# Performance work log

Hardware: AMD Instinct MI355X
Metric: run time of the kernel (lower is better)

The kernel has to match this reference:

```python
import jax, jax.numpy as jnp
import numpy as np

CHUNK = 128
EPS = 1e-6


def setup_inputs() -> dict:
    key = jax.random.key(0)
    k1, k2, k3 = jax.random.split(key, 3)
    B, H, N, D, E = 4, 8, 4096, 64, 64
    q = jax.random.uniform(k1, (B, H, N, D), dtype=jnp.float32)
    k = jax.random.uniform(k2, (B, H, N, D), dtype=jnp.float32)
    v = jax.random.normal(k3, (B, H, N, E), dtype=jnp.float32)
    return {"q": q, "k": k, "v": v, "inferrring_states": 1}


def reference(q, k, v, inferrring_states):
    # infer_hidden_states path: chunked causal linear attention with carried state.
    B, H, N, D = q.shape
    E = v.shape[-1]
    nc = N // CHUNK
    # [nc, B, H, CHUNK, *] for scan over chunks
    qc = jnp.moveaxis(q.reshape(B, H, nc, CHUNK, D), 2, 0)
    kc = jnp.moveaxis(k.reshape(B, H, nc, CHUNK, D), 2, 0)
    vc = jnp.moveaxis(v.reshape(B, H, nc, CHUNK, E), 2, 0)

    Z0 = jnp.zeros((B, H, 1, D), dtype=q.dtype)        # running sum of k
    S0 = jnp.zeros((B, H, 1, D, E), dtype=q.dtype)     # running sum of k v^T

    def step(carry, qkv):
        Z, S = carry
        qi, ki, vi = qkv
        k_cumsum = Z + jnp.cumsum(ki, axis=-2)                      # [B,H,C,D]
        D_inv = 1.0 / jnp.einsum('bhnd,bhnd->bhn', qi, k_cumsum + EPS)
        context = jnp.einsum('bhnd,bhne->bhnde', ki, vi)            # [B,H,C,D,E]
        ctx_cumsum = S + jnp.cumsum(context, axis=-3)
        out = jnp.einsum('bhnde,bhnd,bhn->bhne', ctx_cumsum, qi, D_inv)
        new_carry = (k_cumsum[:, :, -1:], ctx_cumsum[:, :, -1:])
        return new_carry, out

    (Z, S), outs = jax.lax.scan(step, (Z0, S0), (qc, kc, vc))
    out = jnp.moveaxis(outs, 0, 2).reshape(B, H, N, E)
    # states: Z=[B,H,D], S=[B,H,D,E]
    return out, Z[:, :, 0], S[:, :, 0]
```

## Files before the change

### kernel.cpp

```cpp
#include <hip/hip_runtime.h>


#define CHUNKSZ 128
#define DD 64
#define EE 64
#define NC 32
#define NBH 32
#define NSEQ 4096
#define EPSV 1e-6f
#define OUT0 (NBH * NSEQ * EE)
#define KV_ELEMS (NBH * NC * DD * EE)

typedef short bf16x8 __attribute__((ext_vector_type(8)));
typedef short bf16x4 __attribute__((ext_vector_type(4)));
typedef float f32x4  __attribute__((ext_vector_type(4)));

__device__ __forceinline__ unsigned short f2bf(float f) {
    union { float f; unsigned u; } x; x.f = f;
    unsigned u = x.u + 0x7FFFu + ((x.u >> 16) & 1u);
    return (unsigned short)(u >> 16);
}
__device__ __forceinline__ float bf2f(unsigned short s) {
    union { unsigned u; float f; } x; x.u = ((unsigned)s) << 16;
    return x.f;
}

__global__ __launch_bounds__(256) void la_phase1(
    const float* __restrict__ k, const float* __restrict__ v,
    unsigned short* __restrict__ kvT, float* __restrict__ ks)
{
    const int blk = blockIdx.x;
    const int bh = blk / NC, c = blk % NC;
    const size_t rowbase = (size_t)bh * NSEQ + (size_t)c * CHUNKSZ;

    __shared__ alignas(16) unsigned short kT[CHUNKSZ * DD];
    __shared__ alignas(16) unsigned short vT[CHUNKSZ * EE];
    __shared__ float ksp[4][DD];

    char* kb = (char*)kT;
    char* vb = (char*)vT;

    const int t = threadIdx.x;
    const int w = t >> 6, l = t & 63;
    const int lg = l >> 4, lm = l & 15;
    const int col = t & 63;

    float kpart = 0.f;
#pragma unroll
    for (int pass = 0; pass < 4; ++pass) {
        const int mg = w + 4 * pass;
        const float* kp = k + (rowbase + mg * 8) * DD + col;
        const float* vp = v + (rowbase + mg * 8) * EE + col;
        float kf[8], vf[8];
#pragma unroll
        for (int j = 0; j < 8; ++j) kf[j] = kp[(size_t)j * DD];
#pragma unroll
        for (int j = 0; j < 8; ++j) vf[j] = vp[(size_t)j * EE];
        bf16x8 ku, vu;
#pragma unroll
        for (int j = 0; j < 8; ++j) {
            kpart += kf[j];
            ku[j] = (short)f2bf(kf[j]);
            vu[j] = (short)f2bf(vf[j]);
        }
        *(bf16x8*)(kb + mg * 1024 + col * 16) = ku;
        *(bf16x8*)(vb + mg * 1024 + col * 16) = vu;
    }
    ksp[w][col] = kpart;
    __syncthreads();

    f32x4 acc[4] = {};
#pragma unroll
    for (int kk = 0; kk < 4; ++kk) {
        bf16x8 aK = *(bf16x8*)(kb + (lg + 4 * kk) * 1024 + (16 * w + lm) * 16);
#pragma unroll
        for (int ei = 0; ei < 4; ++ei) {
            bf16x8 bV = *(bf16x8*)(vb + (lg + 4 * kk) * 1024 + (16 * ei + lm) * 16);
            acc[ei] = __builtin_amdgcn_mfma_f32_16x16x32_bf16(aK, bV, acc[ei], 0, 0, 0);
        }
    }
    unsigned short* kvout = kvT + (size_t)(bh * NC + c) * DD * EE;
#pragma unroll
    for (int ei = 0; ei < 4; ++ei) {
        bf16x4 u;
        u[0] = (short)f2bf(acc[ei][0]); u[1] = (short)f2bf(acc[ei][1]);
        u[2] = (short)f2bf(acc[ei][2]); u[3] = (short)f2bf(acc[ei][3]);
        *(bf16x4*)(kvout + (16 * ei + lm) * DD + 16 * w + 4 * lg) = u;
    }
    if (t < DD)
        ks[(size_t)(bh * NC + c) * DD + t] = ksp[0][t] + ksp[1][t] + ksp[2][t] + ksp[3][t];
}

__global__ __launch_bounds__(64) void la_phase2(
    unsigned short* __restrict__ kvT, float* __restrict__ ks, float* __restrict__ out)
{
    const int bid = blockIdx.x, t = threadIdx.x;
    if (bid < 256) {
        const int gid = bid * 64 + t;
        const int bh = gid >> 9;
        const int g = gid & 511;
        unsigned short* base = kvT + (size_t)bh * (NC * DD * EE) + (size_t)g * 8;
        bf16x8 vals[NC];
#pragma unroll
        for (int c = 0; c < NC; ++c)
            vals[c] = *(const bf16x8*)(base + (size_t)c * (DD * EE));
        float run[8] = {};
#pragma unroll
        for (int c = 0; c < NC; ++c) {
            bf16x8 pr;
#pragma unroll
            for (int j = 0; j < 8; ++j) pr[j] = (short)f2bf(run[j]);
            *(bf16x8*)(base + (size_t)c * (DD * EE)) = pr;
#pragma unroll
            for (int j = 0; j < 8; ++j) run[j] += bf2f((unsigned short)vals[c][j]);
        }
        const int e = g >> 3, d0 = (g & 7) * 8;
        float* Sout = out + OUT0 + NBH * DD + (size_t)bh * DD * EE;
#pragma unroll
        for (int j = 0; j < 8; ++j)
            Sout[(size_t)(d0 + j) * EE + e] = run[j];
    } else {
        const int tid = (bid - 256) * 64 + t;
        const int bh = tid >> 6, d = tid & 63;
        float vals[NC];
#pragma unroll
        for (int c = 0; c < NC; ++c)
            vals[c] = ks[(size_t)(bh * NC + c) * DD + d];
        float run = 0.f;
#pragma unroll
        for (int c = 0; c < NC; ++c) {
            float x = vals[c];
            ks[(size_t)(bh * NC + c) * DD + d] = run;
            run += x;
        }
        out[OUT0 + tid] = run;
    }
}

__global__ __launch_bounds__(256) void la_phase3(
    const float* __restrict__ q, const float* __restrict__ k,
    const float* __restrict__ v, const unsigned short* __restrict__ kvT,
    const float* __restrict__ ks, float* __restrict__ out)
{
    const int blk = blockIdx.x;
    const int bh = blk / NC, c = blk % NC;
    const size_t rowbase = (size_t)bh * NSEQ + (size_t)c * CHUNKSZ;

    __shared__ alignas(16) unsigned short k_lds[CHUNKSZ * DD];
    __shared__ alignas(16) unsigned short v_lds[CHUNKSZ * EE];
    __shared__ float zi_lds[DD];

    char* kb = (char*)k_lds;
    char* vb = (char*)v_lds;

    const int t  = threadIdx.x;
    const int w  = t >> 6;
    const int l  = t & 63;
    const int lg = l >> 4;
    const int lm = l & 15;

    {
        const float4* kg = (const float4*)(k + rowbase * DD);
#pragma unroll
        for (int i = 0; i < 8; ++i) {
            int idx = t + i * 256;
            int m = idx >> 4, c4 = idx & 15;
            float4 f = kg[idx];
            bf16x4 u;
            u[0] = (short)f2bf(f.x); u[1] = (short)f2bf(f.y);
            u[2] = (short)f2bf(f.z); u[3] = (short)f2bf(f.w);
            int byt = m * 128 + ((c4 * 8) ^ ((m & 7) << 4));
            *(bf16x4*)(kb + byt) = u;
        }
    }
    {
        const int col = t & 63;
#pragma unroll
        for (int pass = 0; pass < 4; ++pass) {
            const int mg = (t >> 6) + 4 * pass;
            const float* vp = v + (rowbase + mg * 8) * EE + col;
            float vf[8];
#pragma unroll
            for (int j = 0; j < 8; ++j) vf[j] = vp[(size_t)j * EE];
            bf16x8 u;
#pragma unroll
            for (int j = 0; j < 8; ++j) u[j] = (short)f2bf(vf[j]);
            *(bf16x8*)(vb + mg * 1024 + col * 16) = u;
        }
    }
    const unsigned short* stc = kvT + (size_t)(bh * NC + c) * DD * EE;
    bf16x8 b_st[4][2];
#pragma unroll
    for (int ei = 0; ei < 4; ++ei)
#pragma unroll
        for (int kk = 0; kk < 2; ++kk)
            b_st[ei][kk] = *(const bf16x8*)(stc + (size_t)(16 * ei + lm) * DD + 8 * lg + 32 * kk);

    if (t < DD) zi_lds[t] = ks[(size_t)(bh * NC + c) * DD + t];
    __syncthreads();

    const int src1 = 32 * (lg & 1) + lm;
    const int src2 = src1 + 16;
    const int par  = lg >> 1;

#pragma unroll
    for (int ni2 = 0; ni2 < 2; ++ni2) {
        const int ni = ni2 ? (7 - w) : w;
        const int n = 16 * ni + lm;
        const int kmax = (ni >> 1) + 1;

        bf16x8 aq[2];
        {
            const float* qrow = q + (rowbase + n) * DD;
#pragma unroll
            for (int kk = 0; kk < 2; ++kk) {
                const float4* p = (const float4*)(qrow + 8 * lg + 32 * kk);
                float4 f0 = p[0], f1 = p[1];
                bf16x8 u;
                u[0] = (short)f2bf(f0.x); u[1] = (short)f2bf(f0.y);
                u[2] = (short)f2bf(f0.z); u[3] = (short)f2bf(f0.w);
                u[4] = (short)f2bf(f1.x); u[5] = (short)f2bf(f1.y);
                u[6] = (short)f2bf(f1.z); u[7] = (short)f2bf(f1.w);
                aq[kk] = u;
            }
        }

        unsigned a_s[4][4];
#pragma unroll
        for (int b = 0; b < 4; ++b) {
            a_s[b][0] = 0; a_s[b][1] = 0; a_s[b][2] = 0; a_s[b][3] = 0;
        }

        float rsum = 0.f;
#pragma unroll
        for (int mi = 0; mi < 8; ++mi) {
            if (mi <= ni) {
                f32x4 cc = {0.f, 0.f, 0.f, 0.f};
                const int mrow = 16 * mi + lm;
#pragma unroll
                for (int kk = 0; kk < 2; ++kk) {
                    int byt = mrow * 128 + (((8 * lg + 32 * kk) * 2) ^ ((mrow & 7) << 4));
                    bf16x8 ak = *(bf16x8*)(kb + byt);
                    cc = __builtin_amdgcn_mfma_f32_16x16x32_bf16(ak, aq[kk], cc, 0, 0, 0);
                }
                const int m0 = 16 * mi + 4 * lg;
                float v0 = (m0 + 0 <= n) ? cc[0] : 0.f;
                float v1 = (m0 + 1 <= n) ? cc[1] : 0.f;
                float v2 = (m0 + 2 <= n) ? cc[2] : 0.f;
                float v3 = (m0 + 3 <= n) ? cc[3] : 0.f;
                rsum += (v0 + v1) + (v2 + v3);
                unsigned p_lo = (unsigned)f2bf(v0) | ((unsigned)f2bf(v1) << 16);
                unsigned p_hi = (unsigned)f2bf(v2) | ((unsigned)f2bf(v3) << 16);
                unsigned w0 = (unsigned)__shfl((int)p_lo, src1);
                unsigned w1 = (unsigned)__shfl((int)p_hi, src1);
                unsigned w2 = (unsigned)__shfl((int)p_lo, src2);
                unsigned w3 = (unsigned)__shfl((int)p_hi, src2);
                const bool take = (par == (mi & 1));
                const int b = mi >> 1;
                a_s[b][0] = take ? w0 : a_s[b][0];
                a_s[b][1] = take ? w1 : a_s[b][1];
                a_s[b][2] = take ? w2 : a_s[b][2];
                a_s[b][3] = take ? w3 : a_s[b][3];
            }
        }

        float qz = 0.f, qs = 0.f;
#pragma unroll
        for (int kk = 0; kk < 2; ++kk) {
#pragma unroll
            for (int i = 0; i < 8; ++i) {
                float qf = bf2f((unsigned short)aq[kk][i]);
                qz += qf * zi_lds[8 * lg + 32 * kk + i];
                qs += qf;
            }
        }
        float part = rsum + qz + EPSV * qs;
        part += __shfl_xor(part, 16);
        part += __shfl_xor(part, 32);
        const float dinv = 1.f / part;

        f32x4 acc[4];
#pragma unroll
        for (int ei = 0; ei < 4; ++ei) {
            f32x4 cc = {0.f, 0.f, 0.f, 0.f};
            const int e = 16 * ei + lm;
            cc = __builtin_amdgcn_mfma_f32_16x16x32_bf16(aq[0], b_st[ei][0], cc, 0, 0, 0);
            cc = __builtin_amdgcn_mfma_f32_16x16x32_bf16(aq[1], b_st[ei][1], cc, 0, 0, 0);
#pragma unroll
            for (int kk = 0; kk < 4; ++kk) {
                if (kk < kmax) {
                    union { unsigned u[4]; bf16x8 f; } as;
                    as.u[0] = a_s[kk][0]; as.u[1] = a_s[kk][1];
                    as.u[2] = a_s[kk][2]; as.u[3] = a_s[kk][3];
                    int bytB = (lg + 4 * kk) * 1024 + e * 16;
                    bf16x8 bv = *(bf16x8*)(vb + bytB);
                    cc = __builtin_amdgcn_mfma_f32_16x16x32_bf16(as.f, bv, cc, 0, 0, 0);
                }
            }
            acc[ei] = cc;
        }

#pragma unroll
        for (int r = 0; r < 4; ++r) {
            float dr = __shfl(dinv, 4 * lg + r);
            const int nr = 16 * ni + 4 * lg + r;
            float* orow = out + (rowbase + nr) * EE + lm;
#pragma unroll
            for (int ei = 0; ei < 4; ++ei)
                orow[16 * ei] = acc[ei][r] * dr;
        }
    }
}

extern "C" void kernel_launch(void* const* d_in, const int* in_sizes, int n_in,
                              void* d_out, int out_size, void* d_ws, size_t ws_size,
                              hipStream_t stream)
{
    (void)in_sizes; (void)n_in; (void)out_size; (void)ws_size;
    const float* q = (const float*)d_in[0];
    const float* k = (const float*)d_in[1];
    const float* v = (const float*)d_in[2];
    float* out = (float*)d_out;
    unsigned short* kvT = (unsigned short*)d_ws;
    float* ks = (float*)(kvT + KV_ELEMS);

    la_phase1<<<NBH * NC, 256, 0, stream>>>(k, v, kvT, ks);
    la_phase2<<<288, 64, 0, stream>>>(kvT, ks, out);
    la_phase3<<<NBH * NC, 256, 0, stream>>>(q, k, v, kvT, ks, out);
}
```

Baseline: 48.78 us.

## Fuse three linear-attention phases into one kernel with atomic-counter inter-block sync

Replaces the three launches with a single persistent-style kernel of 512 blocks, each handling two (bh, chunk) pairs. Blocks compute their chunk's K^T V and k-sum, publish them, and signal an atomic counter per bh. Each block then spin-waits until all chunks of its bh are published and computes its exclusive prefix state by summing the earlier chunks itself. K and V stay in LDS across phases instead of being reloaded. This removes launch gaps, the separate scan pass and the reload of K and V. In exchange it adds O(c) redundant prefix reads per block and relies on all 512 blocks being co-resident to avoid deadlock in the spin-wait.

```diff
diff --git a/kernel.cpp b/kernel.cpp
--- a/kernel.cpp
+++ b/kernel.cpp
@@ -25,133 +25,19 @@
     return x.f;
 }
 
-__global__ __launch_bounds__(256) void la_phase1(
-    const float* __restrict__ k, const float* __restrict__ v,
-    unsigned short* __restrict__ kvT, float* __restrict__ ks)
+__global__ __launch_bounds__(256, 2) void la_fused(
+    const float* __restrict__ q, const float* __restrict__ k,
+    const float* __restrict__ v, unsigned short* __restrict__ kvT,
+    float* __restrict__ ks, int* __restrict__ cnt, float* __restrict__ out)
 {
-    const int blk = blockIdx.x;
-    const int bh = blk / NC, c = blk % NC;
-    const size_t rowbase = (size_t)bh * NSEQ + (size_t)c * CHUNKSZ;
-
-    __shared__ alignas(16) unsigned short kT[CHUNKSZ * DD];
-    __shared__ alignas(16) unsigned short vT[CHUNKSZ * EE];
-    __shared__ float ksp[4][DD];
-
-    char* kb = (char*)kT;
-    char* vb = (char*)vT;
-
-    const int t = threadIdx.x;
-    const int w = t >> 6, l = t & 63;
-    const int lg = l >> 4, lm = l & 15;
-    const int col = t & 63;
-
-    float kpart = 0.f;
-#pragma unroll
-    for (int pass = 0; pass < 4; ++pass) {
-        const int mg = w + 4 * pass;
-        const float* kp = k + (rowbase + mg * 8) * DD + col;
-        const float* vp = v + (rowbase + mg * 8) * EE + col;
-        float kf[8], vf[8];
-#pragma unroll
-        for (int j = 0; j < 8; ++j) kf[j] = kp[(size_t)j * DD];
-#pragma unroll
-        for (int j = 0; j < 8; ++j) vf[j] = vp[(size_t)j * EE];
-        bf16x8 ku, vu;
-#pragma unroll
-        for (int j = 0; j < 8; ++j) {
-            kpart += kf[j];
-            ku[j] = (short)f2bf(kf[j]);
-            vu[j] = (short)f2bf(vf[j]);
-        }
-        *(bf16x8*)(kb + mg * 1024 + col * 16) = ku;
-        *(bf16x8*)(vb + mg * 1024 + col * 16) = vu;
-    }
-    ksp[w][col] = kpart;
-    __syncthreads();
-
-    f32x4 acc[4] = {};
-#pragma unroll
-    for (int kk = 0; kk < 4; ++kk) {
-        bf16x8 aK = *(bf16x8*)(kb + (lg + 4 * kk) * 1024 + (16 * w + lm) * 16);
-#pragma unroll
-        for (int ei = 0; ei < 4; ++ei) {
-            bf16x8 bV = *(bf16x8*)(vb + (lg + 4 * kk) * 1024 + (16 * ei + lm) * 16);
-            acc[ei] = __builtin_amdgcn_mfma_f32_16x16x32_bf16(aK, bV, acc[ei], 0, 0, 0);
-        }
-    }
-    unsigned short* kvout = kvT + (size_t)(bh * NC + c) * DD * EE;
-#pragma unroll
-    for (int ei = 0; ei < 4; ++ei) {
-        bf16x4 u;
-        u[0] = (short)f2bf(acc[ei][0]); u[1] = (short)f2bf(acc[ei][1]);
-        u[2] = (short)f2bf(acc[ei][2]); u[3] = (short)f2bf(acc[ei][3]);
-        *(bf16x4*)(kvout + (16 * ei + lm) * DD + 16 * w + 4 * lg) = u;
-    }
-    if (t < DD)
-        ks[(size_t)(bh * NC + c) * DD + t] = ksp[0][t] + ksp[1][t] + ksp[2][t] + ksp[3][t];
-}
-
-__global__ __launch_bounds__(64) void la_phase2(
-    unsigned short* __restrict__ kvT, float* __restrict__ ks, float* __restrict__ out)
-{
-    const int bid = blockIdx.x, t = threadIdx.x;
-    if (bid < 256) {
-        const int gid = bid * 64 + t;
-        const int bh = gid >> 9;
-        const int g = gid & 511;
-        unsigned short* base = kvT + (size_t)bh * (NC * DD * EE) + (size_t)g * 8;
-        bf16x8 vals[NC];
-#pragma unroll
-        for (int c = 0; c < NC; ++c)
-            vals[c] = *(const bf16x8*)(base + (size_t)c * (DD * EE));
-        float run[8] = {};
-#pragma unroll
-        for (int c = 0; c < NC; ++c) {
-            bf16x8 pr;
-#pragma unroll
-            for (int j = 0; j < 8; ++j) pr[j] = (short)f2bf(run[j]);
-            *(bf16x8*)(base + (size_t)c * (DD * EE)) = pr;
-#pragma unroll
-            for (int j = 0; j < 8; ++j) run[j] += bf2f((unsigned short)vals[c][j]);
-        }
-        const int e = g >> 3, d0 = (g & 7) * 8;
-        float* Sout = out + OUT0 + NBH * DD + (size_t)bh * DD * EE;
-#pragma unroll
-        for (int j = 0; j < 8; ++j)
-            Sout[(size_t)(d0 + j) * EE + e] = run[j];
-    } else {
-        const int tid = (bid - 256) * 64 + t;
-        const int bh = tid >> 6, d = tid & 63;
-        float vals[NC];
-#pragma unroll
-        for (int c = 0; c < NC; ++c)
-            vals[c] = ks[(size_t)(bh * NC + c) * DD + d];
-        float run = 0.f;
-#pragma unroll
-        for (int c = 0; c < NC; ++c) {
-            float x = vals[c];
-            ks[(size_t)(bh * NC + c) * DD + d] = run;
-            run += x;
-        }
-        out[OUT0 + tid] = run;
-    }
-}
-
-__global__ __launch_bounds__(256) void la_phase3(
-    const float* __restrict__ q, const float* __restrict__ k,
-    const float* __restrict__ v, const unsigned short* __restrict__ kvT,
-    const float* __restrict__ ks, float* __restrict__ out)
-{
-    const int blk = blockIdx.x;
-    const int bh = blk / NC, c = blk % NC;
-    const size_t rowbase = (size_t)bh * NSEQ + (size_t)c * CHUNKSZ;
-
-    __shared__ alignas(16) unsigned short k_lds[CHUNKSZ * DD];
-    __shared__ alignas(16) unsigned short v_lds[CHUNKSZ * EE];
+    const int b   = blockIdx.x;
+    const int c   = b & 31;
+    const int bh0 = b >> 5;
+
+    __shared__ alignas(16) unsigned short k_lds[2][CHUNKSZ * DD];
+    __shared__ alignas(16) unsigned short v_lds[2][CHUNKSZ * EE];
+    __shared__ alignas(16) unsigned short st_lds[DD * EE];
     __shared__ float zi_lds[DD];
-
-    char* kb = (char*)k_lds;
-    char* vb = (char*)v_lds;
 
     const int t  = threadIdx.x;
     const int w  = t >> 6;
@@ -159,155 +45,281 @@
     const int lg = l >> 4;
     const int lm = l & 15;
 
-    {
-        const float4* kg = (const float4*)(k + rowbase * DD);
-#pragma unroll
-        for (int i = 0; i < 8; ++i) {
-            int idx = t + i * 256;
-            int m = idx >> 4, c4 = idx & 15;
-            float4 f = kg[idx];
+#pragma unroll
+    for (int s = 0; s < 2; ++s) {
+        const int bh = bh0 + 16 * s;
+        const size_t rowbase = (size_t)bh * NSEQ + (size_t)c * CHUNKSZ;
+        char* kb = (char*)k_lds[s];
+        char* vb = (char*)v_lds[s];
+
+        bf16x8 akf[4];
+        {
+            const int d = 16 * w + lm;
+            const float* kp = k + rowbase * DD + d;
+            float ksum = 0.f;
+#pragma unroll
+            for (int p = 0; p < 4; ++p) {
+                const int mg = lg + 4 * p;
+                float kf[8];
+#pragma unroll
+                for (int j = 0; j < 8; ++j) kf[j] = kp[(size_t)(mg * 8 + j) * DD];
+                bf16x8 u;
+#pragma unroll
+                for (int j = 0; j < 8; ++j) { ksum += kf[j]; u[j] = (short)f2bf(kf[j]); }
+                akf[p] = u;
+#pragma unroll
+                for (int j = 0; j < 8; ++j) {
+                    int m = mg * 8 + j;
+                    *(unsigned short*)(kb + m * 128 + ((2 * d) ^ ((m & 7) << 4))) =
+                        (unsigned short)u[j];
+                }
+            }
+            ksum += __shfl_xor(ksum, 16);
+            ksum += __shfl_xor(ksum, 32);
+            if (lg == 0) ks[(size_t)(bh * NC + c) * DD + d] = ksum;
+        }
+        {
+            const float* vp = v + rowbase * EE + l;
+#pragma unroll
+            for (int p = 0; p < 4; ++p) {
+                const int mg = w + 4 * p;
+                float vf[8];
+#pragma unroll
+                for (int j = 0; j < 8; ++j) vf[j] = vp[(size_t)(mg * 8 + j) * EE];
+                bf16x8 u;
+#pragma unroll
+                for (int j = 0; j < 8; ++j) u[j] = (short)f2bf(vf[j]);
+                *(bf16x8*)(vb + mg * 1024 + l * 16) = u;
+            }
+        }
+        __syncthreads();
+
+        f32x4 acc[4] = {};
+#pragma unroll
+        for (int kk = 0; kk < 4; ++kk) {
+#pragma unroll
+            for (int ei = 0; ei < 4; ++ei) {
+                bf16x8 bV = *(bf16x8*)(vb + (lg + 4 * kk) * 1024 + (16 * ei + lm) * 16);
+                acc[ei] = __builtin_amdgcn_mfma_f32_16x16x32_bf16(akf[kk], bV, acc[ei], 0, 0, 0);
+            }
+        }
+        unsigned short* kvout = kvT + (size_t)(bh * NC + c) * DD * EE;
+#pragma unroll
+        for (int ei = 0; ei < 4; ++ei) {
             bf16x4 u;
-            u[0] = (short)f2bf(f.x); u[1] = (short)f2bf(f.y);
-            u[2] = (short)f2bf(f.z); u[3] = (short)f2bf(f.w);
-            int byt = m * 128 + ((c4 * 8) ^ ((m & 7) << 4));
-            *(bf16x4*)(kb + byt) = u;
+            u[0] = (short)f2bf(acc[ei][0]); u[1] = (short)f2bf(acc[ei][1]);
+            u[2] = (short)f2bf(acc[ei][2]); u[3] = (short)f2bf(acc[ei][3]);
+            *(bf16x4*)(kvout + (16 * ei + lm) * DD + 16 * w + 4 * lg) = u;
+        }
+        __syncthreads();
+        if (t == 0) {
+            __builtin_amdgcn_fence(__ATOMIC_RELEASE, "agent");
+            atomicAdd(&cnt[bh], 1);
         }
     }
-    {
-        const int col = t & 63;
-#pragma unroll
-        for (int pass = 0; pass < 4; ++pass) {
-            const int mg = (t >> 6) + 4 * pass;
-            const float* vp = v + (rowbase + mg * 8) * EE + col;
-            float vf[8];
-#pragma unroll
-            for (int j = 0; j < 8; ++j) vf[j] = vp[(size_t)j * EE];
-            bf16x8 u;
-#pragma unroll
-            for (int j = 0; j < 8; ++j) u[j] = (short)f2bf(vf[j]);
-            *(bf16x8*)(vb + mg * 1024 + col * 16) = u;
-        }
-    }
-    const unsigned short* stc = kvT + (size_t)(bh * NC + c) * DD * EE;
-    bf16x8 b_st[4][2];
-#pragma unroll
-    for (int ei = 0; ei < 4; ++ei)
-#pragma unroll
-        for (int kk = 0; kk < 2; ++kk)
-            b_st[ei][kk] = *(const bf16x8*)(stc + (size_t)(16 * ei + lm) * DD + 8 * lg + 32 * kk);
-
-    if (t < DD) zi_lds[t] = ks[(size_t)(bh * NC + c) * DD + t];
-    __syncthreads();
 
     const int src1 = 32 * (lg & 1) + lm;
     const int src2 = src1 + 16;
     const int par  = lg >> 1;
 
 #pragma unroll
-    for (int ni2 = 0; ni2 < 2; ++ni2) {
-        const int ni = ni2 ? (7 - w) : w;
-        const int n = 16 * ni + lm;
-        const int kmax = (ni >> 1) + 1;
-
-        bf16x8 aq[2];
+    for (int s = 0; s < 2; ++s) {
+        const int bh = bh0 + 16 * s;
+        const size_t rowbase = (size_t)bh * NSEQ + (size_t)c * CHUNKSZ;
+        char* kb  = (char*)k_lds[s];
+        char* vb  = (char*)v_lds[s];
+        char* stb = (char*)st_lds;
+
+        if (t == 0) {
+            while (__hip_atomic_load(cnt + bh, __ATOMIC_RELAXED,
+                                     __HIP_MEMORY_SCOPE_AGENT) < NC)
+                __builtin_amdgcn_s_sleep(8);
+        }
+        __syncthreads();
+        __builtin_amdgcn_fence(__ATOMIC_ACQUIRE, "agent");
+
+        if (t < DD) {
+            const float* kp = ks + (size_t)bh * NC * DD + t;
+            float z = 0.f;
+            for (int j = 0; j < c; ++j) z += kp[(size_t)j * DD];
+            zi_lds[t] = z;
+            if (c == NC - 1)
+                out[OUT0 + (size_t)bh * DD + t] = z + kp[(size_t)(NC - 1) * DD];
+        }
+        float stacc[16];
+#pragma unroll
+        for (int u = 0; u < 16; ++u) stacc[u] = 0.f;
         {
-            const float* qrow = q + (rowbase + n) * DD;
+            const unsigned short* tp = kvT + (size_t)bh * NC * DD * EE + (size_t)t * 16;
+            int j = 0;
+            for (; j + 4 <= c; j += 4) {
+                bf16x8 a0 = *(const bf16x8*)(tp + (size_t)(j + 0) * DD * EE);
+                bf16x8 b0 = *(const bf16x8*)(tp + (size_t)(j + 0) * DD * EE + 8);
+                bf16x8 a1 = *(const bf16x8*)(tp + (size_t)(j + 1) * DD * EE);
+                bf16x8 b1 = *(const bf16x8*)(tp + (size_t)(j + 1) * DD * EE + 8);
+                bf16x8 a2 = *(const bf16x8*)(tp + (size_t)(j + 2) * DD * EE);
+                bf16x8 b2 = *(const bf16x8*)(tp + (size_t)(j + 2) * DD * EE + 8);
+                bf16x8 a3 = *(const bf16x8*)(tp + (size_t)(j + 3) * DD * EE);
+                bf16x8 b3 = *(const bf16x8*)(tp + (size_t)(j + 3) * DD * EE + 8);
+#pragma unroll
+                for (int u = 0; u < 8; ++u) {
+                    stacc[u]     += bf2f((unsigned short)a0[u]) + bf2f((unsigned short)a1[u])
+                                  + bf2f((unsigned short)a2[u]) + bf2f((unsigned short)a3[u]);
+                    stacc[8 + u] += bf2f((unsigned short)b0[u]) + bf2f((unsigned short)b1[u])
+                                  + bf2f((unsigned short)b2[u]) + bf2f((unsigned short)b3[u]);
+                }
+            }
+            for (; j < c; ++j) {
+                bf16x8 a = *(const bf16x8*)(tp + (size_t)j * DD * EE);
+                bf16x8 bb = *(const bf16x8*)(tp + (size_t)j * DD * EE + 8);
+#pragma unroll
+                for (int u = 0; u < 8; ++u) {
+                    stacc[u]     += bf2f((unsigned short)a[u]);
+                    stacc[8 + u] += bf2f((unsigned short)bb[u]);
+                }
+            }
+        }
+        {
+            const int e = t >> 2, d0 = (t & 3) * 16;
+            bf16x8 u0, u1;
+#pragma unroll
+            for (int u = 0; u < 8; ++u) {
+                u0[u] = (short)f2bf(stacc[u]);
+                u1[u] = (short)f2bf(stacc[8 + u]);
+            }
+            *(bf16x8*)(stb + e * 128 + ((2 * d0) ^ ((e & 7) << 4)))       = u0;
+            *(bf16x8*)(stb + e * 128 + ((2 * (d0 + 8)) ^ ((e & 7) << 4))) = u1;
+        }
+        if (c == NC - 1) {
+            const unsigned short* own = kvT + ((size_t)bh * NC + NC - 1) * DD * EE + (size_t)t * 16;
+            bf16x8 a = *(const bf16x8*)own;
+            bf16x8 bb = *(const bf16x8*)(own + 8);
+            const int e = t >> 2, d0 = (t & 3) * 16;
+            float* Sout = out + OUT0 + NBH * DD + (size_t)bh * DD * EE;
+#pragma unroll
+            for (int u = 0; u < 8; ++u)
+                Sout[(size_t)(d0 + u) * EE + e] = stacc[u] + bf2f((unsigned short)a[u]);
+#pragma unroll
+            for (int u = 0; u < 8; ++u)
+                Sout[(size_t)(d0 + 8 + u) * EE + e] = stacc[8 + u] + bf2f((unsigned short)bb[u]);
+        }
+        __syncthreads();
+
+        bf16x8 b_st[4][2];
+#pragma unroll
+        for (int ei = 0; ei < 4; ++ei)
 #pragma unroll
             for (int kk = 0; kk < 2; ++kk) {
-                const float4* p = (const float4*)(qrow + 8 * lg + 32 * kk);
-                float4 f0 = p[0], f1 = p[1];
-                bf16x8 u;
-                u[0] = (short)f2bf(f0.x); u[1] = (short)f2bf(f0.y);
-                u[2] = (short)f2bf(f0.z); u[3] = (short)f2bf(f0.w);
-                u[4] = (short)f2bf(f1.x); u[5] = (short)f2bf(f1.y);
-                u[6] = (short)f2bf(f1.z); u[7] = (short)f2bf(f1.w);
-                aq[kk] = u;
-            }
-        }
-
-        unsigned a_s[4][4];
-#pragma unroll
-        for (int b = 0; b < 4; ++b) {
-            a_s[b][0] = 0; a_s[b][1] = 0; a_s[b][2] = 0; a_s[b][3] = 0;
-        }
-
-        float rsum = 0.f;
-#pragma unroll
-        for (int mi = 0; mi < 8; ++mi) {
-            if (mi <= ni) {
+                int e = 16 * ei + lm;
+                b_st[ei][kk] = *(bf16x8*)(stb + e * 128 + (((8 * lg + 32 * kk) * 2) ^ ((e & 7) << 4)));
+            }
+
+#pragma unroll
+        for (int ni2 = 0; ni2 < 2; ++ni2) {
+            const int ni = ni2 ? (7 - w) : w;
+            const int n = 16 * ni + lm;
+            const int kmax = (ni >> 1) + 1;
+
+            bf16x8 aq[2];
+            {
+                const float* qrow = q + (rowbase + n) * DD;
+#pragma unroll
+                for (int kk = 0; kk < 2; ++kk) {
+                    const float4* p = (const float4*)(qrow + 8 * lg + 32 * kk);
+                    float4 f0 = p[0], f1 = p[1];
+                    bf16x8 u;
+                    u[0] = (short)f2bf(f0.x); u[1] = (short)f2bf(f0.y);
+                    u[2] = (short)f2bf(f0.z); u[3] = (short)f2bf(f0.w);
+                    u[4] = (short)f2bf(f1.x); u[5] = (short)f2bf(f1.y);
+                    u[6] = (short)f2bf(f1.z); u[7] = (short)f2bf(f1.w);
+                    aq[kk] = u;
+                }
+            }
+
+            unsigned a_s[4][4];
+#pragma unroll
+            for (int bb = 0; bb < 4; ++bb) {
+                a_s[bb][0] = 0; a_s[bb][1] = 0; a_s[bb][2] = 0; a_s[bb][3] = 0;
+            }
+
+            float rsum = 0.f;
+#pragma unroll
+            for (int mi = 0; mi < 8; ++mi) {
+                if (mi <= ni) {
+                    f32x4 cc = {0.f, 0.f, 0.f, 0.f};
+                    const int mrow = 16 * mi + lm;
+#pragma unroll
+                    for (int kk = 0; kk < 2; ++kk) {
+                        int byt = mrow * 128 + (((8 * lg + 32 * kk) * 2) ^ ((mrow & 7) << 4));
+                        bf16x8 ak = *(bf16x8*)(kb + byt);
+                        cc = __builtin_amdgcn_mfma_f32_16x16x32_bf16(ak, aq[kk], cc, 0, 0, 0);
+                    }
+                    const int m0 = 16 * mi + 4 * lg;
+                    float v0 = (m0 + 0 <= n) ? cc[0] : 0.f;
+                    float v1 = (m0 + 1 <= n) ? cc[1] : 0.f;
+                    float v2 = (m0 + 2 <= n) ? cc[2] : 0.f;
+                    float v3 = (m0 + 3 <= n) ? cc[3] : 0.f;
+                    rsum += (v0 + v1) + (v2 + v3);
+                    unsigned p_lo = (unsigned)f2bf(v0) | ((unsigned)f2bf(v1) << 16);
+                    unsigned p_hi = (unsigned)f2bf(v2) | ((unsigned)f2bf(v3) << 16);
+                    unsigned w0 = (unsigned)__shfl((int)p_lo, src1);
+                    unsigned w1 = (unsigned)__shfl((int)p_hi, src1);
+                    unsigned w2 = (unsigned)__shfl((int)p_lo, src2);
+                    unsigned w3 = (unsigned)__shfl((int)p_hi, src2);
+                    const bool take = (par == (mi & 1));
+                    const int bb = mi >> 1;
+                    a_s[bb][0] = take ? w0 : a_s[bb][0];
+                    a_s[bb][1] = take ? w1 : a_s[bb][1];
+                    a_s[bb][2] = take ? w2 : a_s[bb][2];
+                    a_s[bb][3] = take ? w3 : a_s[bb][3];
+                }
+            }
+
+            float qz = 0.f, qs = 0.f;
+#pragma unroll
+            for (int kk = 0; kk < 2; ++kk) {
+#pragma unroll
+                for (int i = 0; i < 8; ++i) {
+                    float qf = bf2f((unsigned short)aq[kk][i]);
+                    qz += qf * zi_lds[8 * lg + 32 * kk + i];
+                    qs += qf;
+                }
+            }
+            float part = rsum + qz + EPSV * qs;
+            part += __shfl_xor(part, 16);
+            part += __shfl_xor(part, 32);
+            const float dinv = 1.f / part;
+
+            f32x4 acc3[4];
+#pragma unroll
+            for (int ei = 0; ei < 4; ++ei) {
                 f32x4 cc = {0.f, 0.f, 0.f, 0.f};
-                const int mrow = 16 * mi + lm;
-#pragma unroll
-                for (int kk = 0; kk < 2; ++kk) {
-                    int byt = mrow * 128 + (((8 * lg + 32 * kk) * 2) ^ ((mrow & 7) << 4));
-                    bf16x8 ak = *(bf16x8*)(kb + byt);
-                    cc = __builtin_amdgcn_mfma_f32_16x16x32_bf16(ak, aq[kk], cc, 0, 0, 0);
-                }
-                const int m0 = 16 * mi + 4 * lg;
-                float v0 = (m0 + 0 <= n) ? cc[0] : 0.f;
-                float v1 = (m0 + 1 <= n) ? cc[1] : 0.f;
-                float v2 = (m0 + 2 <= n) ? cc[2] : 0.f;
-                float v3 = (m0 + 3 <= n) ? cc[3] : 0.f;
-                rsum += (v0 + v1) + (v2 + v3);
-                unsigned p_lo = (unsigned)f2bf(v0) | ((unsigned)f2bf(v1) << 16);
-                unsigned p_hi = (unsigned)f2bf(v2) | ((unsigned)f2bf(v3) << 16);
-                unsigned w0 = (unsigned)__shfl((int)p_lo, src1);
-                unsigned w1 = (unsigned)__shfl((int)p_hi, src1);
-                unsigned w2 = (unsigned)__shfl((int)p_lo, src2);
-                unsigned w3 = (unsigned)__shfl((int)p_hi, src2);
-                const bool take = (par == (mi & 1));
-                const int b = mi >> 1;
-                a_s[b][0] = take ? w0 : a_s[b][0];
-                a_s[b][1] = take ? w1 : a_s[b][1];
-                a_s[b][2] = take ? w2 : a_s[b][2];
-                a_s[b][3] = take ? w3 : a_s[b][3];
-            }
-        }
-
-        float qz = 0.f, qs = 0.f;
-#pragma unroll
-        for (int kk = 0; kk < 2; ++kk) {
-#pragma unroll
-            for (int i = 0; i < 8; ++i) {
-                float qf = bf2f((unsigned short)aq[kk][i]);
-                qz += qf * zi_lds[8 * lg + 32 * kk + i];
-                qs += qf;
-            }
-        }
-        float part = rsum + qz + EPSV * qs;
-        part += __shfl_xor(part, 16);
-        part += __shfl_xor(part, 32);
-        const float dinv = 1.f / part;
-
-        f32x4 acc[4];
-#pragma unroll
-        for (int ei = 0; ei < 4; ++ei) {
-            f32x4 cc = {0.f, 0.f, 0.f, 0.f};
-            const int e = 16 * ei + lm;
-            cc = __builtin_amdgcn_mfma_f32_16x16x32_bf16(aq[0], b_st[ei][0], cc, 0, 0, 0);
-            cc = __builtin_amdgcn_mfma_f32_16x16x32_bf16(aq[1], b_st[ei][1], cc, 0, 0, 0);
-#pragma unroll
-            for (int kk = 0; kk < 4; ++kk) {
-                if (kk < kmax) {
-                    union { unsigned u[4]; bf16x8 f; } as;
-                    as.u[0] = a_s[kk][0]; as.u[1] = a_s[kk][1];
-                    as.u[2] = a_s[kk][2]; as.u[3] = a_s[kk][3];
-                    int bytB = (lg + 4 * kk) * 1024 + e * 16;
-                    bf16x8 bv = *(bf16x8*)(vb + bytB);
-                    cc = __builtin_amdgcn_mfma_f32_16x16x32_bf16(as.f, bv, cc, 0, 0, 0);
-                }
-            }
-            acc[ei] = cc;
-        }
-
-#pragma unroll
-        for (int r = 0; r < 4; ++r) {
-            float dr = __shfl(dinv, 4 * lg + r);
-            const int nr = 16 * ni + 4 * lg + r;
-            float* orow = out + (rowbase + nr) * EE + lm;
-#pragma unroll
-            for (int ei = 0; ei < 4; ++ei)
-                orow[16 * ei] = acc[ei][r] * dr;
+                const int e = 16 * ei + lm;
+                cc = __builtin_amdgcn_mfma_f32_16x16x32_bf16(aq[0], b_st[ei][0], cc, 0, 0, 0);
+                cc = __builtin_amdgcn_mfma_f32_16x16x32_bf16(aq[1], b_st[ei][1], cc, 0, 0, 0);
+#pragma unroll
+                for (int kk = 0; kk < 4; ++kk) {
+                    if (kk < kmax) {
+                        union { unsigned u[4]; bf16x8 f; } as;
+                        as.u[0] = a_s[kk][0]; as.u[1] = a_s[kk][1];
+                        as.u[2] = a_s[kk][2]; as.u[3] = a_s[kk][3];
+                        int bytB = (lg + 4 * kk) * 1024 + e * 16;
+                        bf16x8 bv = *(bf16x8*)(vb + bytB);
+                        cc = __builtin_amdgcn_mfma_f32_16x16x32_bf16(as.f, bv, cc, 0, 0, 0);
+                    }
+                }
+                acc3[ei] = cc;
+            }
+
+#pragma unroll
+            for (int r = 0; r < 4; ++r) {
+                float dr = __shfl(dinv, 4 * lg + r);
+                const int nr = 16 * ni + 4 * lg + r;
+                float* orow = out + (rowbase + nr) * EE + lm;
+#pragma unroll
+                for (int ei = 0; ei < 4; ++ei)
+                    orow[16 * ei] = acc3[ei][r] * dr;
+            }
         }
     }
 }
@@ -323,8 +335,8 @@
     float* out = (float*)d_out;
     unsigned short* kvT = (unsigned short*)d_ws;
     float* ks = (float*)(kvT + KV_ELEMS);
-
-    la_phase1<<<NBH * NC, 256, 0, stream>>>(k, v, kvT, ks);
-    la_phase2<<<288, 64, 0, stream>>>(kvT, ks, out);
-    la_phase3<<<NBH * NC, 256, 0, stream>>>(q, k, v, kvT, ks, out);
+    int* cnt = (int*)(ks + NBH * NC * DD);
+
+    hipMemsetAsync(cnt, 0, NBH * sizeof(int), stream);
+    la_fused<<<512, 256, 0, stream>>>(q, k, v, kvT, ks, cnt, out);
 }
```

After: 122.9 us, median of 2. 152% more time.
